# Performance work log

Hardware: AMD Instinct MI355X
Metric: run time of the kernel (lower is better)

The kernel has to match this reference:

```python
import jax, jax.numpy as jnp
import numpy as np
import math

B, F, NB, H1, H2, K = 16384, 64, 64, 128, 128, 3
LN_EPS = 1e-5


def setup_inputs() -> dict:
    key = jax.random.key(0)
    ks = jax.random.split(key, 16)
    x = jax.random.normal(ks[0], (B, F), dtype=jnp.float32)
    # RBF params (per feature): centers init linspace(-3,3), log_widths = log(step)
    centers = jnp.broadcast_to(jnp.linspace(-3.0, 3.0, NB), (F, NB)).astype(jnp.float32)
    step = 6.0 / (NB - 1)
    log_widths = jnp.full((F, NB), math.log(step), dtype=jnp.float32)
    def lin(k, shape, fan_in):
        return jax.random.normal(k, shape, dtype=jnp.float32) / np.sqrt(fan_in)
    W1 = lin(ks[1], (F, NB, H1), NB); b1 = jnp.zeros((F, H1), jnp.float32)
    g1 = jnp.ones((F, H1), jnp.float32); be1 = jnp.zeros((F, H1), jnp.float32)
    W2 = lin(ks[2], (F, H1, H2), H1); b2 = jnp.zeros((F, H2), jnp.float32)
    g2 = jnp.ones((F, H2), jnp.float32); be2 = jnp.zeros((F, H2), jnp.float32)
    Wr = lin(ks[3], (F, NB, H2), NB); br = jnp.zeros((F, H2), jnp.float32)
    att = jnp.zeros((F,), jnp.float32)
    bias = jnp.zeros((H2,), jnp.float32)
    Wpi = lin(ks[4], (H2, K), H2); bpi = jnp.zeros((K,), jnp.float32)
    Wa = lin(ks[5], (H2, K), H2); ba = jnp.zeros((K,), jnp.float32)
    Wb = lin(ks[6], (H2, K), H2); bb = jnp.zeros((K,), jnp.float32)
    return dict(x=x, centers=centers, log_widths=log_widths, W1=W1, b1=b1, g1=g1,
                be1=be1, W2=W2, b2=b2, g2=g2, be2=be2, Wr=Wr, br=br, att=att,
                bias=bias, Wpi=Wpi, bpi=bpi, Wa=Wa, ba=ba, Wb=Wb, bb=bb)


def _layernorm(h, g, b):
    mu = jnp.mean(h, axis=-1, keepdims=True)
    var = jnp.mean((h - mu) ** 2, axis=-1, keepdims=True)
    return (h - mu) * jax.lax.rsqrt(var + LN_EPS) * g + b


def reference(x, centers, log_widths, W1, b1, g1, be1, W2, b2, g2, be2, Wr, br,
              att, bias, Wpi, bpi, Wa, ba, Wb, bb):
    # RBF expansion, feature axis batched: x [B,F] -> [B,F,NB]
    xc = jnp.clip(x, -10.0, 10.0)
    widths = jnp.exp(jnp.clip(log_widths, -5.0, 5.0)) + 0.1  # [F,NB]
    dist = (xc[:, :, None] - centers[None]) / widths[None]
    rbf = jnp.exp(-0.5 * jnp.clip(dist, -10.0, 10.0) ** 2)  # [B,F,NB]
    # per-feature MLP (grouped GEMMs via einsum)
    h = jnp.einsum('bfn,fnh->bfh', rbf, W1) + b1[None]
    h = jax.nn.gelu(_layernorm(h, g1[None], be1[None]), approximate=False)
    h = jnp.einsum('bfh,fhk->bfk', h, W2) + b2[None]
    h = jax.nn.gelu(_layernorm(h, g2[None], be2[None]), approximate=False)
    res = jnp.einsum('bfn,fnh->bfh', rbf, Wr) + br[None]
    stacked = h + 0.1 * res  # [B,F,H2]
    # attention-weighted aggregation over features
    w = jax.nn.softmax(att)
    agg = jnp.einsum('bfh,f->bh', stacked, w) + bias  # [B,H2]
    # mixture-beta head
    pi = jax.nn.softmax(agg @ Wpi + bpi, axis=-1)
    alpha = jnp.clip(jax.nn.softplus(agg @ Wa + ba) + 1.01, 1.01, 100.0)
    beta = jnp.clip(jax.nn.softplus(agg @ Wb + bb) + 1.01, 1.01, 100.0)
    pred = jnp.sum(pi * (alpha / (alpha + beta)), axis=-1)
    return jnp.clip(pred, 0.001, 0.999)
```

## Files before the change

kernel.cpp:

```cpp
#include <hip/hip_runtime.h>
#include <math.h>

#define BQ   16384
#define FQ   64
#define NBQ  64
#define HD   128
#define FG   4
#define FPG  16
#define MT   128
#define NT   512

typedef __attribute__((ext_vector_type(8))) short s16x8;
typedef __attribute__((ext_vector_type(4))) float f32x4;

__device__ __forceinline__ unsigned short f2bf(float x) {
    unsigned int u = __float_as_uint(x);
    return (unsigned short)((u + 0x7FFFu + ((u >> 16) & 1u)) >> 16);
}
__device__ __forceinline__ unsigned short bftr(float x) {
    return (unsigned short)(__float_as_uint(x) >> 16);
}

__device__ __forceinline__ float softplus_stable(float v) {
    return (v > 0.0f) ? (v + log1pf(expf(-v))) : log1pf(expf(v));
}

__device__ __forceinline__ f32x4 gelu4(f32x4 v) {
    const f32x4 v2 = v * v;
    const f32x4 tt = v2 * (-0.07135481f) + (-1.5957691f);
    const f32x4 s  = v * tt;
    f32x4 r;
    r[0] = __fdividef(v[0], 1.0f + __expf(s[0]));
    r[1] = __fdividef(v[1], 1.0f + __expf(s[1]));
    r[2] = __fdividef(v[2], 1.0f + __expf(s[2]));
    r[3] = __fdividef(v[3], 1.0f + __expf(s[3]));
    return r;
}

__device__ __forceinline__ float dppsum16(float x) {
    int t;
    t = __builtin_amdgcn_update_dpp(0, __float_as_int(x), 0xB1,  0xF, 0xF, true);
    x += __int_as_float(t);
    t = __builtin_amdgcn_update_dpp(0, __float_as_int(x), 0x4E,  0xF, 0xF, true);
    x += __int_as_float(t);
    t = __builtin_amdgcn_update_dpp(0, __float_as_int(x), 0x125, 0xF, 0xF, true);
    x += __int_as_float(t);
    t = __builtin_amdgcn_update_dpp(0, __float_as_int(x), 0x129, 0xF, 0xF, true);
    x += __int_as_float(t);
    return x;
}

__device__ __forceinline__ void load16_lds(const unsigned short* g, unsigned short* l) {
    __builtin_amdgcn_global_load_lds(
        (const __attribute__((address_space(1))) unsigned int*)(uintptr_t)g,
        (__attribute__((address_space(3))) unsigned int*)(uintptr_t)l,
        16, 0, 0);
}

__device__ __forceinline__ int hofs(int row, int col) {
    return row * 128 + (col ^ (((row >> 2) & 3) << 4));
}

__global__ void __launch_bounds__(256) prep_all(
    const float* __restrict__ x,
    const float* __restrict__ att, const float* __restrict__ log_widths,
    const float* __restrict__ centers, const float* __restrict__ br,
    const float* __restrict__ bias,
    const float* __restrict__ W1, const float* __restrict__ Wr, const float* __restrict__ W2,
    const float* __restrict__ b1, const float* __restrict__ g1, const float* __restrict__ be1,
    const float* __restrict__ b2, const float* __restrict__ g2, const float* __restrict__ be2,
    unsigned short* __restrict__ W1s, unsigned short* __restrict__ Wrs,
    unsigned short* __restrict__ W2s,
    float* __restrict__ xT,
    float* __restrict__ wsoft, float* __restrict__ crw2, float* __restrict__ rbias,
    float* __restrict__ Pk)
{
    const int bid = blockIdx.x;
    const int t   = threadIdx.x;

    if (bid < 1024) {
        const int gid = bid * 256 + t;
        const float* W; unsigned short* dst; int K, id;
        if (gid < 65536)       { W = W1; dst = W1s; K = 64;  id = gid; }
        else if (gid < 131072) { W = Wr; dst = Wrs; K = 64;  id = gid - 65536; }
        else                   { W = W2; dst = W2s; K = 128; id = gid - 131072; }
        const int KB = K >> 3;
        const int nn = id & 15;
        const int kb = (id >> 4) % KB;
        const int nt = ((id >> 4) / KB) & 7;
        const int f  = id / (KB * 16 * 8);
        const float* src = W + ((size_t)f * K + kb * 8) * HD + nt * 16 + nn;
        s16x8 o;
#pragma unroll
        for (int j = 0; j < 8; ++j) o[j] = (short)f2bf(src[(size_t)j * HD]);
        *(s16x8*)(dst + (size_t)f * K * HD + ((size_t)(nt * KB + kb) * 16 + nn) * 8) = o;
    } else if (bid < 1280) {
        __shared__ float tile[64][65];
        const int b0 = (bid - 1024) * 64;
        {
            const int row = t & 63, cg = (t >> 6) * 16;
            const float4* src = (const float4*)(x + (size_t)(b0 + row) * FQ + cg);
#pragma unroll
            for (int i = 0; i < 4; ++i) {
                const float4 v = src[i];
                tile[row][cg + i * 4 + 0] = v.x;
                tile[row][cg + i * 4 + 1] = v.y;
                tile[row][cg + i * 4 + 2] = v.z;
                tile[row][cg + i * 4 + 3] = v.w;
            }
        }
        __syncthreads();
        {
            const int f = t >> 2, r0 = (t & 3) * 16;
            float* dst = xT + (size_t)f * BQ + b0 + r0;
#pragma unroll
            for (int i = 0; i < 16; ++i) dst[i] = tile[r0 + i][f];
        }
    } else if (bid == 1280) {
        __shared__ float ws[64];
        if (t < 64) {
            float v = att[t];
            float m = v;
#pragma unroll
            for (int s = 32; s >= 1; s >>= 1) m = fmaxf(m, __shfl_xor(m, s, 64));
            float e = expf(v - m);
            float ssum = e;
#pragma unroll
            for (int s = 32; s >= 1; s >>= 1) ssum += __shfl_xor(ssum, s, 64);
            const float w = e / ssum;
            ws[t] = w;
            wsoft[t] = w;
        }
        __syncthreads();
        for (int i = t; i < FQ * NBQ; i += 256) {
            float lw = fminf(fmaxf(log_widths[i], -5.0f), 5.0f);
            const float rw = 1.0f / (expf(lw) + 0.1f);
            ((float2*)crw2)[i] = make_float2(rw, -centers[i] * rw);
        }
        if (t < HD) {
            float s = bias[t];
            for (int f = 0; f < FQ; ++f) s += 0.1f * ws[f] * br[f * HD + t];
            rbias[t] = s;
        }
    } else {
        const int id = (bid - 1281) * 256 + t;
        if (id < FQ * HD) {
            ((float4*)Pk)[id * 2]     = make_float4(b1[id], g1[id], be1[id], 0.0f);
            ((float4*)Pk)[id * 2 + 1] = make_float4(b2[id], g2[id], be2[id], 0.0f);
        }
    }
}

__global__ void __launch_bounds__(NT, 4) nam_main(
    const float* __restrict__ crw2,
    const float* __restrict__ xT,
    const unsigned short* __restrict__ W1s,
    const unsigned short* __restrict__ Wrs,
    const unsigned short* __restrict__ W2s,
    const float* __restrict__ Pk,
    const float* __restrict__ wsoft,
    float* __restrict__ aggP)
{
    __shared__ __align__(16) unsigned short wbuf[16384];
    __shared__ __align__(16) unsigned short hbuf[16384];

    const int t    = threadIdx.x;
    const int ln   = t & 63;
    const int wv   = t >> 6;
    const int n    = ln & 15;
    const int q    = ln >> 4;
    const int wrow = wv * 16;
    const int fg   = blockIdx.x & 3;
    const int rb   = blockIdx.x >> 2;
    const int b0   = rb * MT;

    f32x4 acc[8];
#pragma unroll
    for (int nt = 0; nt < 8; ++nt) acc[nt] = f32x4{0.f, 0.f, 0.f, 0.f};

    {
        const int f0 = fg * FPG + (rb & (FPG - 1));
        const unsigned short* gw1 = W1s + (size_t)f0 * 8192;
        const unsigned short* gwr = Wrs + (size_t)f0 * 8192;
#pragma unroll
        for (int i = 0; i < 4; ++i) {
            const int chunk = i * 8 + wv;
            const unsigned short* src = (chunk < 16) ? (gw1 + chunk * 512)
                                                     : (gwr + (chunk - 16) * 512);
            load16_lds(src + ln * 8, wbuf + chunk * 512);
        }
    }

    int4 pf0, pf1, pf2, pf3;

    for (int ff = 0; ff < FPG; ++ff) {
        const int f = fg * FPG + ((ff + rb) & (FPG - 1));

        if (ff > 0) {
            *(int4*)&wbuf[t * 8]         = pf0;
            *(int4*)&wbuf[4096 + t * 8]  = pf1;
            *(int4*)&wbuf[8192 + t * 8]  = pf2;
            *(int4*)&wbuf[12288 + t * 8] = pf3;
        }

        s16x8 a0, a1;
        {
            float xv = xT[(size_t)f * BQ + b0 + wrow + n];
            xv = fminf(fmaxf(xv, -10.0f), 10.0f);
            const float4* c4 = ((const float4*)crw2) + f * 32;
            unsigned int p[8];
#pragma unroll
            for (int h = 0; h < 2; ++h) {
#pragma unroll
                for (int i = 0; i < 4; ++i) {
                    const float4 cc = c4[h * 16 + q * 4 + i];
                    const float d0 = fmaf(xv, cc.x, cc.y);
                    const float d1 = fmaf(xv, cc.z, cc.w);
                    const float e0 = __expf(-0.5f * d0 * d0);
                    const float e1 = __expf(-0.5f * d1 * d1);
                    p[h * 4 + i] = __builtin_amdgcn_perm(__float_as_uint(e1),
                                                         __float_as_uint(e0), 0x07060302u);
                }
            }
            int4 pa = make_int4(p[0], p[1], p[2], p[3]);
            int4 pb = make_int4(p[4], p[5], p[6], p[7]);
            a0 = *(s16x8*)&pa;
            a1 = *(s16x8*)&pb;
        }
        const float wf   = wsoft[f];
        const float wf01 = 0.1f * wf;
        __syncthreads();

        {
            const int f2 = fg * FPG + ((ff + 1 + rb) & (FPG - 1));
            const unsigned short* g1p = W1s + (size_t)f2 * 8192 + t * 8;
            const unsigned short* grp = Wrs + (size_t)f2 * 8192 + t * 8;
            pf0 = *(const int4*)(g1p);
            pf1 = *(const int4*)(g1p + 4096);
            pf2 = *(const int4*)(grp);
            pf3 = *(const int4*)(grp + 4096);
        }

        f32x4 hc[8];
#pragma unroll
        for (int nt = 0; nt < 8; ++nt) {
            const s16x8 bA = *(const s16x8*)&wbuf[(nt * 8 + 0) * 128 + ln * 8];
            const s16x8 bB = *(const s16x8*)&wbuf[(nt * 8 + 4) * 128 + ln * 8];
            f32x4 z = f32x4{0.f, 0.f, 0.f, 0.f};
            z = __builtin_amdgcn_mfma_f32_16x16x32_bf16(a0, bA, z, 0, 0, 0);
            z = __builtin_amdgcn_mfma_f32_16x16x32_bf16(a1, bB, z, 0, 0, 0);
            hc[nt] = z;
            const s16x8 cA = *(const s16x8*)&wbuf[8192 + (nt * 8 + 0) * 128 + ln * 8];
            const s16x8 cB = *(const s16x8*)&wbuf[8192 + (nt * 8 + 4) * 128 + ln * 8];
            f32x4 y = f32x4{0.f, 0.f, 0.f, 0.f};
            y = __builtin_amdgcn_mfma_f32_16x16x32_bf16(a0, cA, y, 0, 0, 0);
            y = __builtin_amdgcn_mfma_f32_16x16x32_bf16(a1, cB, y, 0, 0, 0);
            acc[nt] = y * wf01 + acc[nt];
        }
        __syncthreads();

        {
            const unsigned short* gw2 = W2s + (size_t)f * 16384;
#pragma unroll
            for (int i = 0; i < 4; ++i) {
                const int chunk = i * 8 + wv;
                load16_lds(gw2 + chunk * 512 + ln * 8, wbuf + chunk * 512);
            }
        }

        const size_t pkb = ((size_t)f * HD + n) * 8;
        f32x4 sm = {0.f, 0.f, 0.f, 0.f}, sq = {0.f, 0.f, 0.f, 0.f};
#pragma unroll
        for (int nt = 0; nt < 8; ++nt) {
            const float4 pA = *(const float4*)(Pk + pkb + nt * 128);
            const f32x4 v = hc[nt] + pA.x;
            hc[nt] = v; sm += v; sq += v * v;
        }
        f32x4 mu4, rs4;
#pragma unroll
        for (int i = 0; i < 4; ++i) {
            const float s  = dppsum16(sm[i]);
            const float qq = dppsum16(sq[i]);
            mu4[i] = s * (1.0f / 128.0f);
            const float var = qq * (1.0f / 128.0f) - mu4[i] * mu4[i];
            rs4[i] = rsqrtf(var + 1e-5f);
        }
#pragma unroll
        for (int nt = 0; nt < 8; ++nt) {
            const float4 pA = *(const float4*)(Pk + pkb + nt * 128);
            const f32x4 sg = rs4 * pA.y;
            const f32x4 c1 = -mu4 * sg + pA.z;
            const f32x4 z  = gelu4(hc[nt] * sg + c1);
#pragma unroll
            for (int i = 0; i < 4; ++i)
                hbuf[hofs(wrow + q * 4 + i, nt * 16 + n)] = bftr(z[i]);
        }
        __syncthreads();

        s16x8 A2[4];
#pragma unroll
        for (int c = 0; c < 4; ++c)
            A2[c] = *(const s16x8*)&hbuf[hofs(wrow + n, c * 32 + q * 8)];
#pragma unroll
        for (int nt = 0; nt < 8; ++nt) {
            f32x4 z = f32x4{0.f, 0.f, 0.f, 0.f};
#pragma unroll
            for (int c = 0; c < 4; ++c) {
                const s16x8 bF = *(const s16x8*)&wbuf[(nt * 16 + c * 4) * 128 + ln * 8];
                z = __builtin_amdgcn_mfma_f32_16x16x32_bf16(A2[c], bF, z, 0, 0, 0);
            }
            hc[nt] = z;
        }

        sm = f32x4{0.f, 0.f, 0.f, 0.f}; sq = f32x4{0.f, 0.f, 0.f, 0.f};
#pragma unroll
        for (int nt = 0; nt < 8; ++nt) {
            const float4 pB = *(const float4*)(Pk + pkb + nt * 128 + 4);
            const f32x4 v = hc[nt] + pB.x;
            hc[nt] = v; sm += v; sq += v * v;
        }
#pragma unroll
        for (int i = 0; i < 4; ++i) {
            const float s  = dppsum16(sm[i]);
            const float qq = dppsum16(sq[i]);
            mu4[i] = s * (1.0f / 128.0f);
            const float var = qq * (1.0f / 128.0f) - mu4[i] * mu4[i];
            rs4[i] = rsqrtf(var + 1e-5f);
        }
#pragma unroll
        for (int nt = 0; nt < 8; ++nt) {
            const float4 pB = *(const float4*)(Pk + pkb + nt * 128 + 4);
            const f32x4 sg = rs4 * pB.y;
            const f32x4 c1 = -mu4 * sg + pB.z;
            acc[nt] = gelu4(hc[nt] * sg + c1) * wf + acc[nt];
        }
        __syncthreads();
    }

    float* ap = aggP + ((size_t)fg * BQ + b0 + wrow + q * 4) * HD + n;
#pragma unroll
    for (int nt = 0; nt < 8; ++nt) {
#pragma unroll
        for (int i = 0; i < 4; ++i) {
            ap[(size_t)i * HD + nt * 16] = acc[nt][i];
        }
    }
}

__global__ void __launch_bounds__(256) nam_head(
    const float* __restrict__ aggP, const float* __restrict__ rbias,
    const float* __restrict__ Wpi, const float* __restrict__ bpi,
    const float* __restrict__ Wa,  const float* __restrict__ ba,
    const float* __restrict__ Wb,  const float* __restrict__ bb,
    float* __restrict__ out)
{
    const int gid  = blockIdx.x * blockDim.x + threadIdx.x;
    const int row  = gid >> 6;
    const int lane = threadIdx.x & 63;
    if (row >= BQ) return;

    const float2 p0 = ((const float2*)(aggP + (size_t)row * HD))[lane];
    const float2 p1 = ((const float2*)(aggP + ((size_t)BQ + row) * HD))[lane];
    const float2 p2 = ((const float2*)(aggP + ((size_t)2 * BQ + row) * HD))[lane];
    const float2 p3 = ((const float2*)(aggP + ((size_t)3 * BQ + row) * HD))[lane];
    const float2 rb = ((const float2*)rbias)[lane];
    const float ax = p0.x + p1.x + p2.x + p3.x + rb.x;
    const float ay = p0.y + p1.y + p2.y + p3.y + rb.y;

    const float2* wp = (const float2*)Wpi;
    const float2* wa = (const float2*)Wa;
    const float2* wb = (const float2*)Wb;
    const float2 p01 = wp[lane * 3], p23 = wp[lane * 3 + 1], p45 = wp[lane * 3 + 2];
    const float2 a01 = wa[lane * 3], a23 = wa[lane * 3 + 1], a45 = wa[lane * 3 + 2];
    const float2 b01 = wb[lane * 3], b23 = wb[lane * 3 + 1], b45 = wb[lane * 3 + 2];

    float ppi0 = ax * p01.x + ay * p23.y;
    float ppi1 = ax * p01.y + ay * p45.x;
    float ppi2 = ax * p23.x + ay * p45.y;
    float pa0  = ax * a01.x + ay * a23.y;
    float pa1  = ax * a01.y + ay * a45.x;
    float pa2  = ax * a23.x + ay * a45.y;
    float pb0  = ax * b01.x + ay * b23.y;
    float pb1  = ax * b01.y + ay * b45.x;
    float pb2  = ax * b23.x + ay * b45.y;

#pragma unroll
    for (int s = 32; s >= 1; s >>= 1) {
        ppi0 += __shfl_xor(ppi0, s, 64);
        ppi1 += __shfl_xor(ppi1, s, 64);
        ppi2 += __shfl_xor(ppi2, s, 64);
        pa0  += __shfl_xor(pa0,  s, 64);
        pa1  += __shfl_xor(pa1,  s, 64);
        pa2  += __shfl_xor(pa2,  s, 64);
        pb0  += __shfl_xor(pb0,  s, 64);
        pb1  += __shfl_xor(pb1,  s, 64);
        pb2  += __shfl_xor(pb2,  s, 64);
    }

    if (lane == 0) {
        const float z0 = ppi0 + bpi[0], z1 = ppi1 + bpi[1], z2 = ppi2 + bpi[2];
        const float mz = fmaxf(z0, fmaxf(z1, z2));
        const float e0 = expf(z0 - mz), e1 = expf(z1 - mz), e2 = expf(z2 - mz);
        const float es = e0 + e1 + e2;

        const float al0 = fminf(fmaxf(softplus_stable(pa0 + ba[0]) + 1.01f, 1.01f), 100.0f);
        const float al1 = fminf(fmaxf(softplus_stable(pa1 + ba[1]) + 1.01f, 1.01f), 100.0f);
        const float al2 = fminf(fmaxf(softplus_stable(pa2 + ba[2]) + 1.01f, 1.01f), 100.0f);
        const float bt0 = fminf(fmaxf(softplus_stable(pb0 + bb[0]) + 1.01f, 1.01f), 100.0f);
        const float bt1 = fminf(fmaxf(softplus_stable(pb1 + bb[1]) + 1.01f, 1.01f), 100.0f);
        const float bt2 = fminf(fmaxf(softplus_stable(pb2 + bb[2]) + 1.01f, 1.01f), 100.0f);

        const float pred = (e0 * (al0 / (al0 + bt0))
                          + e1 * (al1 / (al1 + bt1))
                          + e2 * (al2 / (al2 + bt2))) / es;
        out[row] = fminf(fmaxf(pred, 0.001f), 0.999f);
    }
}

extern "C" void kernel_launch(void* const* d_in, const int* in_sizes, int n_in,
                              void* d_out, int out_size, void* d_ws, size_t ws_size,
                              hipStream_t stream) {
    const float* x          = (const float*)d_in[0];
    const float* centers    = (const float*)d_in[1];
    const float* log_widths = (const float*)d_in[2];
    const float* W1   = (const float*)d_in[3];
    const float* b1   = (const float*)d_in[4];
    const float* g1   = (const float*)d_in[5];
    const float* be1  = (const float*)d_in[6];
    const float* W2   = (const float*)d_in[7];
    const float* b2   = (const float*)d_in[8];
    const float* g2   = (const float*)d_in[9];
    const float* be2  = (const float*)d_in[10];
    const float* Wr   = (const float*)d_in[11];
    const float* br   = (const float*)d_in[12];
    const float* att  = (const float*)d_in[13];
    const float* bias = (const float*)d_in[14];
    const float* Wpi  = (const float*)d_in[15];
    const float* bpi  = (const float*)d_in[16];
    const float* Wa   = (const float*)d_in[17];
    const float* ba   = (const float*)d_in[18];
    const float* Wb   = (const float*)d_in[19];
    const float* bb   = (const float*)d_in[20];

    char* ws = (char*)d_ws;
    float*          wsoft = (float*)(ws + 0);
    float*          rbias = (float*)(ws + 1024);
    float*          crw2  = (float*)(ws + 8192);
    float*          Pk    = (float*)(ws + 65536);
    float*          xT    = (float*)(ws + 327680);
    unsigned short* W1s   = (unsigned short*)(ws + 4521984);
    unsigned short* Wrs   = (unsigned short*)(ws + 5570560);
    unsigned short* W2s   = (unsigned short*)(ws + 6619136);
    float*          aggP  = (float*)(ws + 8716288);

    prep_all<<<1313, 256, 0, stream>>>(x, att, log_widths, centers, br, bias,
                                       W1, Wr, W2, b1, g1, be1, b2, g2, be2,
                                       W1s, Wrs, W2s, xT, wsoft, crw2, rbias, Pk);

    nam_main<<<(BQ / MT) * FG, NT, 0, stream>>>(crw2, xT, W1s, Wrs, W2s, Pk,
                                                wsoft, aggP);

    nam_head<<<BQ / 4, 256, 0, stream>>>(aggP, rbias, Wpi, bpi, Wa, ba, Wb, bb,
                                         (float*)d_out);
}
```

Measured before the change: 464.7 us.

## Ping-pong LDS weight buffers, drop x transpose, restructure weight repack

The main kernel now splits its LDS into two halves that swap roles each feature iteration. The next feature's W1/Wr weights are loaded asynchronously, global-to-LDS, into the half just freed by the hidden activations. This replaces the register prefetch and the end-of-loop barrier. The x transpose pass is removed and x is read directly with a strided access. The weight bf16 repack in prep now goes through a coalesced LDS-staged tile, which uses far fewer blocks. The risks are a strided, uncoalesced x load inside the main loop and the correctness of the barrier placement around the buffer swap.

```diff
diff --git a/kernel.cpp b/kernel.cpp
--- a/kernel.cpp
+++ b/kernel.cpp
@@ -62,7 +62,6 @@
 }
 
 __global__ void __launch_bounds__(256) prep_all(
-    const float* __restrict__ x,
     const float* __restrict__ att, const float* __restrict__ log_widths,
     const float* __restrict__ centers, const float* __restrict__ br,
     const float* __restrict__ bias,
@@ -71,52 +70,48 @@
     const float* __restrict__ b2, const float* __restrict__ g2, const float* __restrict__ be2,
     unsigned short* __restrict__ W1s, unsigned short* __restrict__ Wrs,
     unsigned short* __restrict__ W2s,
-    float* __restrict__ xT,
     float* __restrict__ wsoft, float* __restrict__ crw2, float* __restrict__ rbias,
     float* __restrict__ Pk)
 {
     const int bid = blockIdx.x;
     const int t   = threadIdx.x;
 
-    if (bid < 1024) {
-        const int gid = bid * 256 + t;
-        const float* W; unsigned short* dst; int K, id;
-        if (gid < 65536)       { W = W1; dst = W1s; K = 64;  id = gid; }
-        else if (gid < 131072) { W = Wr; dst = Wrs; K = 64;  id = gid - 65536; }
-        else                   { W = W2; dst = W2s; K = 128; id = gid - 131072; }
-        const int KB = K >> 3;
-        const int nn = id & 15;
-        const int kb = (id >> 4) % KB;
-        const int nt = ((id >> 4) / KB) & 7;
-        const int f  = id / (KB * 16 * 8);
-        const float* src = W + ((size_t)f * K + kb * 8) * HD + nt * 16 + nn;
-        s16x8 o;
-#pragma unroll
-        for (int j = 0; j < 8; ++j) o[j] = (short)f2bf(src[(size_t)j * HD]);
-        *(s16x8*)(dst + (size_t)f * K * HD + ((size_t)(nt * KB + kb) * 16 + nn) * 8) = o;
-    } else if (bid < 1280) {
-        __shared__ float tile[64][65];
-        const int b0 = (bid - 1024) * 64;
-        {
-            const int row = t & 63, cg = (t >> 6) * 16;
-            const float4* src = (const float4*)(x + (size_t)(b0 + row) * FQ + cg);
-#pragma unroll
-            for (int i = 0; i < 4; ++i) {
-                const float4 v = src[i];
-                tile[row][cg + i * 4 + 0] = v.x;
-                tile[row][cg + i * 4 + 1] = v.y;
-                tile[row][cg + i * 4 + 2] = v.z;
-                tile[row][cg + i * 4 + 3] = v.w;
-            }
-        }
-        __syncthreads();
-        {
-            const int f = t >> 2, r0 = (t & 3) * 16;
-            float* dst = xT + (size_t)f * BQ + b0 + r0;
-#pragma unroll
-            for (int i = 0; i < 16; ++i) dst[i] = tile[r0 + i][f];
-        }
-    } else if (bid == 1280) {
+    if (bid < 256) {
+        __shared__ unsigned int tile32[4096];
+        const float* src; unsigned short* dst; int KB, kbase;
+        if (bid < 64)       { src = W1 + (size_t)bid * 8192;        dst = W1s + (size_t)bid * 8192;        KB = 8;  kbase = 0; }
+        else if (bid < 128) { src = Wr + (size_t)(bid - 64) * 8192; dst = Wrs + (size_t)(bid - 64) * 8192; KB = 8;  kbase = 0; }
+        else {
+            const int u = bid - 128, f = u >> 1, half = u & 1;
+            src = W2 + ((size_t)f * 128 + half * 64) * 128;
+            dst = W2s + (size_t)f * 16384;
+            KB = 16; kbase = half * 8;
+        }
+        const float4* src4 = (const float4*)src;
+#pragma unroll
+        for (int i = 0; i < 8; ++i) {
+            const int idx = t + i * 256;
+            const float4 v = src4[idx];
+            const unsigned int u0 = (unsigned int)f2bf(v.x) | ((unsigned int)f2bf(v.y) << 16);
+            const unsigned int u1 = (unsigned int)f2bf(v.z) | ((unsigned int)f2bf(v.w) << 16);
+            tile32[idx * 2]     = u0;
+            tile32[idx * 2 + 1] = u1;
+        }
+        __syncthreads();
+        const unsigned short* tile16 = (const unsigned short*)tile32;
+#pragma unroll
+        for (int i = 0; i < 4; ++i) {
+            const int u  = t + i * 256;
+            const int nn = u & 15;
+            const int kb = (u >> 4) & 7;
+            const int nt = u >> 7;
+            s16x8 o;
+#pragma unroll
+            for (int j = 0; j < 8; ++j)
+                o[j] = (short)tile16[(kb * 8 + j) * 128 + nt * 16 + nn];
+            *(s16x8*)(dst + ((size_t)((nt * KB + kbase + kb) * 16 + nn)) * 8) = o;
+        }
+    } else if (bid == 256) {
         __shared__ float ws[64];
         if (t < 64) {
             float v = att[t];
@@ -143,7 +138,7 @@
             rbias[t] = s;
         }
     } else {
-        const int id = (bid - 1281) * 256 + t;
+        const int id = (bid - 257) * 256 + t;
         if (id < FQ * HD) {
             ((float4*)Pk)[id * 2]     = make_float4(b1[id], g1[id], be1[id], 0.0f);
             ((float4*)Pk)[id * 2 + 1] = make_float4(b2[id], g2[id], be2[id], 0.0f);
@@ -153,7 +148,7 @@
 
 __global__ void __launch_bounds__(NT, 4) nam_main(
     const float* __restrict__ crw2,
-    const float* __restrict__ xT,
+    const float* __restrict__ x,
     const unsigned short* __restrict__ W1s,
     const unsigned short* __restrict__ Wrs,
     const unsigned short* __restrict__ W2s,
@@ -161,8 +156,7 @@
     const float* __restrict__ wsoft,
     float* __restrict__ aggP)
 {
-    __shared__ __align__(16) unsigned short wbuf[16384];
-    __shared__ __align__(16) unsigned short hbuf[16384];
+    __shared__ __align__(16) unsigned short lds[32768];
 
     const int t    = threadIdx.x;
     const int ln   = t & 63;
@@ -187,25 +181,18 @@
             const int chunk = i * 8 + wv;
             const unsigned short* src = (chunk < 16) ? (gw1 + chunk * 512)
                                                      : (gwr + (chunk - 16) * 512);
-            load16_lds(src + ln * 8, wbuf + chunk * 512);
-        }
-    }
-
-    int4 pf0, pf1, pf2, pf3;
+            load16_lds(src + ln * 8, lds + chunk * 512);
+        }
+    }
 
     for (int ff = 0; ff < FPG; ++ff) {
         const int f = fg * FPG + ((ff + rb) & (FPG - 1));
-
-        if (ff > 0) {
-            *(int4*)&wbuf[t * 8]         = pf0;
-            *(int4*)&wbuf[4096 + t * 8]  = pf1;
-            *(int4*)&wbuf[8192 + t * 8]  = pf2;
-            *(int4*)&wbuf[12288 + t * 8] = pf3;
-        }
+        unsigned short* W = lds + ((ff & 1) ? 16384 : 0);
+        unsigned short* H = lds + ((ff & 1) ? 0 : 16384);
 
         s16x8 a0, a1;
         {
-            float xv = xT[(size_t)f * BQ + b0 + wrow + n];
+            float xv = x[(size_t)(b0 + wrow + n) * FQ + f];
             xv = fminf(fmaxf(xv, -10.0f), 10.0f);
             const float4* c4 = ((const float4*)crw2) + f * 32;
             unsigned int p[8];
@@ -231,27 +218,17 @@
         const float wf01 = 0.1f * wf;
         __syncthreads();
 
-        {
-            const int f2 = fg * FPG + ((ff + 1 + rb) & (FPG - 1));
-            const unsigned short* g1p = W1s + (size_t)f2 * 8192 + t * 8;
-            const unsigned short* grp = Wrs + (size_t)f2 * 8192 + t * 8;
-            pf0 = *(const int4*)(g1p);
-            pf1 = *(const int4*)(g1p + 4096);
-            pf2 = *(const int4*)(grp);
-            pf3 = *(const int4*)(grp + 4096);
-        }
-
         f32x4 hc[8];
 #pragma unroll
         for (int nt = 0; nt < 8; ++nt) {
-            const s16x8 bA = *(const s16x8*)&wbuf[(nt * 8 + 0) * 128 + ln * 8];
-            const s16x8 bB = *(const s16x8*)&wbuf[(nt * 8 + 4) * 128 + ln * 8];
+            const s16x8 bA = *(const s16x8*)&W[(nt * 8 + 0) * 128 + ln * 8];
+            const s16x8 bB = *(const s16x8*)&W[(nt * 8 + 4) * 128 + ln * 8];
             f32x4 z = f32x4{0.f, 0.f, 0.f, 0.f};
             z = __builtin_amdgcn_mfma_f32_16x16x32_bf16(a0, bA, z, 0, 0, 0);
             z = __builtin_amdgcn_mfma_f32_16x16x32_bf16(a1, bB, z, 0, 0, 0);
             hc[nt] = z;
-            const s16x8 cA = *(const s16x8*)&wbuf[8192 + (nt * 8 + 0) * 128 + ln * 8];
-            const s16x8 cB = *(const s16x8*)&wbuf[8192 + (nt * 8 + 4) * 128 + ln * 8];
+            const s16x8 cA = *(const s16x8*)&W[8192 + (nt * 8 + 0) * 128 + ln * 8];
+            const s16x8 cB = *(const s16x8*)&W[8192 + (nt * 8 + 4) * 128 + ln * 8];
             f32x4 y = f32x4{0.f, 0.f, 0.f, 0.f};
             y = __builtin_amdgcn_mfma_f32_16x16x32_bf16(a0, cA, y, 0, 0, 0);
             y = __builtin_amdgcn_mfma_f32_16x16x32_bf16(a1, cB, y, 0, 0, 0);
@@ -264,7 +241,7 @@
 #pragma unroll
             for (int i = 0; i < 4; ++i) {
                 const int chunk = i * 8 + wv;
-                load16_lds(gw2 + chunk * 512 + ln * 8, wbuf + chunk * 512);
+                load16_lds(gw2 + chunk * 512 + ln * 8, W + chunk * 512);
             }
         }
 
@@ -293,20 +270,35 @@
             const f32x4 z  = gelu4(hc[nt] * sg + c1);
 #pragma unroll
             for (int i = 0; i < 4; ++i)
-                hbuf[hofs(wrow + q * 4 + i, nt * 16 + n)] = bftr(z[i]);
+                H[hofs(wrow + q * 4 + i, nt * 16 + n)] = bftr(z[i]);
         }
         __syncthreads();
 
         s16x8 A2[4];
 #pragma unroll
         for (int c = 0; c < 4; ++c)
-            A2[c] = *(const s16x8*)&hbuf[hofs(wrow + n, c * 32 + q * 8)];
+            A2[c] = *(const s16x8*)&H[hofs(wrow + n, c * 32 + q * 8)];
+        __syncthreads();
+
+        if (ff + 1 < FPG) {
+            const int f2 = fg * FPG + ((ff + 1 + rb) & (FPG - 1));
+            const unsigned short* gw1 = W1s + (size_t)f2 * 8192;
+            const unsigned short* gwr = Wrs + (size_t)f2 * 8192;
+#pragma unroll
+            for (int i = 0; i < 4; ++i) {
+                const int chunk = i * 8 + wv;
+                const unsigned short* src = (chunk < 16) ? (gw1 + chunk * 512)
+                                                         : (gwr + (chunk - 16) * 512);
+                load16_lds(src + ln * 8, H + chunk * 512);
+            }
+        }
+
 #pragma unroll
         for (int nt = 0; nt < 8; ++nt) {
             f32x4 z = f32x4{0.f, 0.f, 0.f, 0.f};
 #pragma unroll
             for (int c = 0; c < 4; ++c) {
-                const s16x8 bF = *(const s16x8*)&wbuf[(nt * 16 + c * 4) * 128 + ln * 8];
+                const s16x8 bF = *(const s16x8*)&W[(nt * 16 + c * 4) * 128 + ln * 8];
                 z = __builtin_amdgcn_mfma_f32_16x16x32_bf16(A2[c], bF, z, 0, 0, 0);
             }
             hc[nt] = z;
@@ -334,7 +326,6 @@
             const f32x4 c1 = -mu4 * sg + pB.z;
             acc[nt] = gelu4(hc[nt] * sg + c1) * wf + acc[nt];
         }
-        __syncthreads();
     }
 
     float* ap = aggP + ((size_t)fg * BQ + b0 + wrow + q * 4) * HD + n;
@@ -447,17 +438,16 @@
     float*          rbias = (float*)(ws + 1024);
     float*          crw2  = (float*)(ws + 8192);
     float*          Pk    = (float*)(ws + 65536);
-    float*          xT    = (float*)(ws + 327680);
-    unsigned short* W1s   = (unsigned short*)(ws + 4521984);
-    unsigned short* Wrs   = (unsigned short*)(ws + 5570560);
-    unsigned short* W2s   = (unsigned short*)(ws + 6619136);
-    float*          aggP  = (float*)(ws + 8716288);
-
-    prep_all<<<1313, 256, 0, stream>>>(x, att, log_widths, centers, br, bias,
-                                       W1, Wr, W2, b1, g1, be1, b2, g2, be2,
-                                       W1s, Wrs, W2s, xT, wsoft, crw2, rbias, Pk);
-
-    nam_main<<<(BQ / MT) * FG, NT, 0, stream>>>(crw2, xT, W1s, Wrs, W2s, Pk,
+    unsigned short* W1s   = (unsigned short*)(ws + 327680);
+    unsigned short* Wrs   = (unsigned short*)(ws + 1376256);
+    unsigned short* W2s   = (unsigned short*)(ws + 2424832);
+    float*          aggP  = (float*)(ws + 4521984);
+
+    prep_all<<<289, 256, 0, stream>>>(att, log_widths, centers, br, bias,
+                                      W1, Wr, W2, b1, g1, be1, b2, g2, be2,
+                                      W1s, Wrs, W2s, wsoft, crw2, rbias, Pk);
+
+    nam_main<<<(BQ / MT) * FG, NT, 0, stream>>>(crw2, x, W1s, Wrs, W2s, Pk,
                                                 wsoft, aggP);
 
     nam_head<<<BQ / 4, 256, 0, stream>>>(aggP, rbias, Wpi, bpi, Wa, ba, Wb, bb,
```

Result: slower. 556.3 us (+19.7%).
